# Optimization experiments

Measured on AMD Instinct MI355X. Metric: run time of the kernel, lower is better.

## Reference

```python
import jax, jax.numpy as jnp
import numpy as np

DIM = 768
NUM_HEADS = 12
HEAD_DIM = DIM // NUM_HEADS


def setup_inputs() -> dict:
    key = jax.random.key(0)
    k1, k2, k3 = jax.random.split(key, 3)
    B, N, C = 8, 4096, DIM
    x = jax.random.normal(k1, (B, N, C), dtype=jnp.float32)
    # torch nn.Linear weights are (out_features, in_features)
    W_qkv = jax.random.normal(k2, (3 * C, C), dtype=jnp.float32) * 0.02
    b_qkv = jnp.zeros((3 * C,), dtype=jnp.float32)
    W_proj = jax.random.normal(k3, (C, C), dtype=jnp.float32) * 0.02
    b_proj = jnp.zeros((C,), dtype=jnp.float32)
    return {"x": x, "W_qkv": W_qkv, "b_qkv": b_qkv, "W_proj": W_proj, "b_proj": b_proj}


def reference(x, W_qkv, b_qkv, W_proj, b_proj):
    B, N, C = x.shape
    H, D = NUM_HEADS, HEAD_DIM
    # qkv projection -> (3, B, H, N, D)
    qkv = (x @ W_qkv.T + b_qkv).reshape(B, N, 3, H, D).transpose(2, 0, 3, 1, 4)
    q, k, v = qkv[0], qkv[1], qkv[2]
    # feature map: elu(x) + 1 (positive kernel features)
    q = jax.nn.elu(q) + 1.0
    k = jax.nn.elu(k) + 1.0
    # kernelized linear attention: (K^T V) then Q (K^T V)
    kv = jnp.einsum('bhnd,bhnv->bhdv', k, v)          # (B,H,D,D)
    out = jnp.einsum('bhnd,bhdv->bhnv', q, kv)        # (B,H,N,D)
    k_sum = k.sum(axis=2)                             # (B,H,D)
    normalizer = jnp.einsum('bhnd,bhd->bhn', q, k_sum) + 1e-06
    out = out / normalizer[..., None]
    out = out.transpose(0, 2, 1, 3).reshape(B, N, C)
    out = out @ W_proj.T + b_proj
    return out
```

## Files before the change

### kernel.cpp

```cpp
#include <hip/hip_runtime.h>
#include <hip/hip_fp16.h>
#include <math.h>

#define NHEADS 12
#define SEQ 4096
#define BATCH 8

typedef _Float16 half8 __attribute__((ext_vector_type(8)));
typedef float floatx4 __attribute__((ext_vector_type(4)));

__global__ void zero_kernel(float* p, int n) {
  int i = blockIdx.x * 256 + threadIdx.x;
  if (i < n) p[i] = 0.f;
}

__global__ void cast_f2h(const float* __restrict__ in, __half* __restrict__ out, int n) {
  int i = (blockIdx.x * 256 + threadIdx.x) * 4;
  if (i < n) {
    float4 v = *(const float4*)&in[i];
    ushort4 o;
    o.x = __half_as_ushort(__float2half(v.x));
    o.y = __half_as_ushort(__float2half(v.y));
    o.z = __half_as_ushort(__float2half(v.z));
    o.w = __half_as_ushort(__float2half(v.w));
    *(ushort4*)&out[i] = o;
  }
}

__device__ __forceinline__ void stage_tile(const __half* __restrict__ gbase, int ldg,
                                           _Float16* lds, int t) {
#pragma unroll
  for (int it = 0; it < 2; ++it) {
    const int s  = it * 256 + t;
    const int mp = s >> 3, ps = s & 7;
    const int p  = ps ^ (mp & 7);
    const int r  = mp * 2 + (p >> 2);
    const int q  = p & 3;
    const __half* g = gbase + (size_t)r * ldg + q * 8;
    _Float16* dst = lds + (s >> 6) * 512;
    __builtin_amdgcn_global_load_lds((const __attribute__((address_space(1))) void*)g,
                                     (__attribute__((address_space(3))) void*)dst, 16, 0, 0);
  }
}
__device__ __forceinline__ void stage_blk(const __half* __restrict__ gbase, int ldg,
                                          _Float16* lds, int t) {
  const int mp = t >> 3, ps = t & 7;
  const int p  = ps ^ (mp & 7);
  const int r  = mp * 2 + (p >> 2);
  const int q  = p & 3;
  const __half* g = gbase + (size_t)r * ldg + q * 8;
  _Float16* dst = lds + (t >> 6) * 512;
  __builtin_amdgcn_global_load_lds((const __attribute__((address_space(1))) void*)g,
                                   (__attribute__((address_space(3))) void*)dst, 16, 0, 0);
}
__device__ __forceinline__ half8 read_frag(const _Float16* lds, int row, int quad) {
  const int mp = row >> 1;
  const int p  = ((row & 1) << 2) | quad;
  const int ps = p ^ (mp & 7);
  return *(const half8*)(lds + (mp * 8 + ps) * 8);
}

__device__ __forceinline__ void write_l64(_Float16* lds, int row, int col, float v) {
  lds[row * 64 + ((((col >> 3) ^ (row & 7))) << 3) + (col & 7)] = (_Float16)v;
}
__device__ __forceinline__ half8 read_l64c(const _Float16* lds, int row, int c) {
  return *(const half8*)(lds + row * 64 + ((c ^ (row & 7)) << 3));
}

__device__ __forceinline__ void barrier_raw() {
  asm volatile("s_barrier" ::: "memory");
}

template<int MODE>
__global__ __launch_bounds__(512, 2) void hgemm256_kernel(
    const __half* __restrict__ A, const __half* __restrict__ W,
    const float* __restrict__ bias,
    __half* __restrict__ outK, __half* __restrict__ outV,
    float* __restrict__ outF, int colBase)
{
  const int K = 768;
  const int NT = 24;
  extern __shared__ __align__(16) _Float16 sh[];
  const int t    = threadIdx.x;
  const int w    = t >> 6;
  const int l    = t & 63;
  const int quad = l >> 4;
  const int mrow = l & 15;
  const int wm   = w >> 2;
  const int wn   = w & 3;

  constexpr int JB = (MODE == 1) ? 6 : 3;
  const int bid  = blockIdx.x;
  const int xcd  = bid & 7;
  const int ii   = bid >> 3;
  const int mg   = ii / JB;
  const int jj   = ii - mg * JB;
  const int m0   = (xcd * 16 + mg) * 256;
  const int j0   = jj * 256;

  floatx4 acc[8][4];
#pragma unroll
  for (int i = 0; i < 8; ++i)
#pragma unroll
    for (int j = 0; j < 4; ++j) acc[i][j] = (floatx4){0.f, 0.f, 0.f, 0.f};

#pragma unroll
  for (int kt = 0; kt < 3; ++kt) {
    _Float16* db = sh + kt * 16384;
    const int kg = kt * 32;
    stage_blk(A + (size_t)m0 * K + kg, K, db, t);
    stage_blk(A + (size_t)(m0 + 128) * K + kg, K, db + 4096, t);
    stage_blk(W + (size_t)(colBase + j0) * K + kg, K, db + 8192, t);
    stage_blk(W + (size_t)(colBase + j0 + 128) * K + kg, K, db + 12288, t);
  }
  asm volatile("s_waitcnt vmcnt(8)" ::: "memory");
  barrier_raw();

#pragma unroll 4
  for (int kt = 0; kt < NT; ++kt) {
    const _Float16* bb = sh + (kt & 3) * 16384;
    const bool st = (kt + 3 < NT);
    _Float16* db = sh + ((kt + 3) & 3) * 16384;
    const int kg = (kt + 3) * 32;
    half8 af[4], bf[4];

#pragma unroll
    for (int j = 0; j < 4; ++j) {
      const int C = wn * 64 + j * 16 + mrow;
      bf[j] = read_frag(bb + 8192 + (C >> 7) * 4096, C & 127, quad);
    }
#pragma unroll
    for (int i = 0; i < 4; ++i)
      af[i] = read_frag(bb + wm * 4096, i * 16 + mrow, quad);
    if (st) {
      stage_blk(A + (size_t)m0 * K + kg, K, db, t);
      stage_blk(A + (size_t)(m0 + 128) * K + kg, K, db + 4096, t);
    }
#pragma unroll
    for (int i = 0; i < 4; ++i)
#pragma unroll
      for (int j = 0; j < 4; ++j)
        acc[i][j] = __builtin_amdgcn_mfma_f32_16x16x32_f16(af[i], bf[j], acc[i][j], 0, 0, 0);

#pragma unroll
    for (int i = 0; i < 4; ++i)
      af[i] = read_frag(bb + wm * 4096, (i + 4) * 16 + mrow, quad);
    if (st) {
      stage_blk(W + (size_t)(colBase + j0) * K + kg, K, db + 8192, t);
      stage_blk(W + (size_t)(colBase + j0 + 128) * K + kg, K, db + 12288, t);
    }
#pragma unroll
    for (int i = 0; i < 4; ++i)
#pragma unroll
      for (int j = 0; j < 4; ++j)
        acc[i + 4][j] = __builtin_amdgcn_mfma_f32_16x16x32_f16(af[i], bf[j], acc[i + 4][j], 0, 0, 0);

    if (kt < NT - 3)       asm volatile("s_waitcnt vmcnt(8)" ::: "memory");
    else if (kt == NT - 3) asm volatile("s_waitcnt vmcnt(4)" ::: "memory");
    else if (kt == NT - 2) asm volatile("s_waitcnt vmcnt(0)" ::: "memory");
    barrier_raw();
  }

  if (MODE == 0) {
#pragma unroll
    for (int j = 0; j < 4; ++j) {
      const int col = j0 + wn * 64 + j * 16 + mrow;
      const float bsv = bias[col];
#pragma unroll
      for (int i = 0; i < 8; ++i)
#pragma unroll
        for (int r = 0; r < 4; ++r) {
          const int m = m0 + wm * 128 + i * 16 + quad * 4 + r;
          outF[(size_t)m * 768 + col] = acc[i][j][r] + bsv;
        }
    }
    return;
  }

  const int col0 = colBase + j0 + wn * 64;
  const int t3   = col0 / 768;
  const int h    = (col0 - t3 * 768) >> 6;
  __half* dst    = (t3 == 1) ? outK : outV;
  const int m0w  = m0 + wm * 128;
  const int b_   = m0w >> 12;
  const int n0w  = m0w & 4095;
  _Float16* scr  = sh + w * 4096;
  const size_t gbT = (size_t)(b_ * NHEADS + h) * 64 * 4096;

#pragma unroll
  for (int hf = 0; hf < 2; ++hf) {
#pragma unroll
    for (int j = 0; j < 4; ++j) {
      const int col = j * 16 + mrow;
      const float bsv = bias[col0 + col];
#pragma unroll
      for (int ii2 = 0; ii2 < 4; ++ii2)
#pragma unroll
        for (int r = 0; r < 4; ++r) {
          const int row = ii2 * 16 + quad * 4 + r;
          float val = acc[hf * 4 + ii2][j][r] + bsv;
          if (t3 == 1) val = (val > 0.f) ? (val + 1.f) : expf(val);
          write_l64(scr, col, row, val);
        }
    }
    barrier_raw();
#pragma unroll
    for (int it = 0; it < 8; ++it) {
      const int dd = it * 8 + (l >> 3);
      const int c  = l & 7;
      half8 vv = read_l64c(scr, dd, c);
      *(half8*)((_Float16*)dst + gbT + (size_t)dd * 4096 + n0w + hf * 64 + c * 8) = vv;
    }
    barrier_raw();
  }
}

__global__ __launch_bounds__(256) void kv_mfma_kernel(
    const __half* __restrict__ kT, const __half* __restrict__ vT,
    float* __restrict__ kv, float* __restrict__ ksum)
{
  extern __shared__ float red[];
  float* ksr = red + 4 * 4096;
  const int bh = blockIdx.x;
  const int sp = blockIdx.y;
  const int t  = threadIdx.x;
  const int w  = t >> 6;
  const int l  = t & 63;
  const int quad = l >> 4;
  const int mrow = l & 15;
  const size_t base = (size_t)bh * 64 * 4096;
  const int n0 = sp * 1024 + w * 256;

  floatx4 acc[4][4];
  floatx4 ks[4];
#pragma unroll
  for (int i = 0; i < 4; ++i) {
    ks[i] = (floatx4){0.f, 0.f, 0.f, 0.f};
#pragma unroll
    for (int j = 0; j < 4; ++j) acc[i][j] = (floatx4){0.f, 0.f, 0.f, 0.f};
  }
  half8 ones;
#pragma unroll
  for (int e = 0; e < 8; ++e) ones[e] = (_Float16)1.0f;

  const __half* pk[4];
  const __half* pv[4];
#pragma unroll
  for (int i = 0; i < 4; ++i) {
    pk[i] = kT + base + (size_t)(i * 16 + mrow) * 4096 + n0 + quad * 8;
    pv[i] = vT + base + (size_t)(i * 16 + mrow) * 4096 + n0 + quad * 8;
  }

#pragma unroll
  for (int nn = 0; nn < 256; nn += 32) {
    half8 af[4], bf[4];
#pragma unroll
    for (int i = 0; i < 4; ++i) af[i] = *(const half8*)(pk[i] + nn);
#pragma unroll
    for (int j = 0; j < 4; ++j) bf[j] = *(const half8*)(pv[j] + nn);
#pragma unroll
    for (int i = 0; i < 4; ++i)
#pragma unroll
      for (int j = 0; j < 4; ++j)
        acc[i][j] = __builtin_amdgcn_mfma_f32_16x16x32_f16(af[i], bf[j], acc[i][j], 0, 0, 0);
#pragma unroll
    for (int i = 0; i < 4; ++i)
      ks[i] = __builtin_amdgcn_mfma_f32_16x16x32_f16(af[i], ones, ks[i], 0, 0, 0);
  }

  float* rw = red + w * 4096;
#pragma unroll
  for (int i = 0; i < 4; ++i)
#pragma unroll
    for (int j = 0; j < 4; ++j)
#pragma unroll
      for (int r = 0; r < 4; ++r)
        rw[(i * 16 + quad * 4 + r) * 64 + j * 16 + mrow] = acc[i][j][r];
  if (mrow == 0) {
#pragma unroll
    for (int i = 0; i < 4; ++i)
#pragma unroll
      for (int r = 0; r < 4; ++r)
        ksr[w * 64 + i * 16 + quad * 4 + r] = ks[i][r];
  }
  __syncthreads();
#pragma unroll
  for (int ii = 0; ii < 16; ++ii) {
    const int idx = ii * 256 + t;
    const float s = red[idx] + red[4096 + idx] + red[8192 + idx] + red[12288 + idx];
    atomicAdd(&kv[(size_t)bh * 4096 + idx], s);
  }
  if (t < 64)
    atomicAdd(&ksum[(size_t)bh * 64 + t], ksr[t] + ksr[64 + t] + ksr[128 + t] + ksr[192 + t]);
}

__global__ __launch_bounds__(256) void qattn_kernel(
    const __half* __restrict__ A, const __half* __restrict__ W,
    const float* __restrict__ bias,
    const float* __restrict__ kvg, const float* __restrict__ ksumg,
    __half* __restrict__ att)
{
  const int K = 768;
  __shared__ __align__(16) _Float16 sh[24576];
  _Float16* As = sh;
  _Float16* Bs = sh + 4096;
  __shared__ float norms[256];
  __shared__ float ksums[128];
  const int t    = threadIdx.x;
  const int w    = t >> 6;
  const int l    = t & 63;
  const int quad = l >> 4;
  const int mrow = l & 15;
  const int m0   = blockIdx.x * 128;
  const int j0   = blockIdx.y * 128;
  const int wr   = (w >> 1) * 64;
  const int wc   = (w & 1) * 64;
  const int b_   = m0 >> 12;
  const int h0   = j0 >> 6;

  {
    _Float16* kvT0 = sh + 16384;
#pragma unroll
    for (int ii = 0; ii < 32; ++ii) {
      const int gidx = ii * 256 + t;
      const int head = gidx >> 12;
      const int r    = gidx & 4095;
      const float val = kvg[(size_t)(b_ * NHEADS + h0 + head) * 4096 + r];
      write_l64(kvT0 + head * 4096, r & 63, r >> 6, val);
    }
    if (t < 128) ksums[t] = ksumg[(size_t)(b_ * NHEADS + h0 + (t >> 6)) * 64 + (t & 63)];
  }

  floatx4 acc[4][4];
#pragma unroll
  for (int i = 0; i < 4; ++i)
#pragma unroll
    for (int j = 0; j < 4; ++j) acc[i][j] = (floatx4){0.f, 0.f, 0.f, 0.f};

  for (int k0 = 0; k0 < K; k0 += 32) {
    __syncthreads();
    stage_tile(A + (size_t)m0 * K + k0, K, As, t);
    stage_tile(W + (size_t)j0 * K + k0, K, Bs, t);
    __syncthreads();
    half8 af[4], bf[4];
#pragma unroll
    for (int i = 0; i < 4; ++i) af[i] = read_frag(As, wr + i * 16 + mrow, quad);
#pragma unroll
    for (int j = 0; j < 4; ++j) bf[j] = read_frag(Bs, wc + j * 16 + mrow, quad);
#pragma unroll
    for (int i = 0; i < 4; ++i)
#pragma unroll
      for (int j = 0; j < 4; ++j)
        acc[i][j] = __builtin_amdgcn_mfma_f32_16x16x32_f16(af[i], bf[j], acc[i][j], 0, 0, 0);
  }

  _Float16* qtile = sh + w * 4096;
  const _Float16* kvT = sh + 16384 + (w & 1) * 4096;
  const int hh = w & 1;

  __syncthreads();
#pragma unroll
  for (int j = 0; j < 4; ++j) {
    const int col = j * 16 + mrow;
    const float bsv = bias[j0 + wc + col];
#pragma unroll
    for (int i = 0; i < 4; ++i)
#pragma unroll
      for (int r = 0; r < 4; ++r) {
        const int row = i * 16 + quad * 4 + r;
        float val = acc[i][j][r] + bsv;
        val = (val > 0.f) ? (val + 1.f) : expf(val);
        write_l64(qtile, row, col, val);
      }
  }
  __syncthreads();

  {
    float nrm = 0.f;
#pragma unroll
    for (int c = 0; c < 8; ++c) {
      half8 qv = read_l64c(qtile, l, c);
#pragma unroll
      for (int e = 0; e < 8; ++e) nrm += (float)qv[e] * ksums[hh * 64 + c * 8 + e];
    }
    norms[w * 64 + l] = 1.f / (nrm + 1e-6f);
  }

  floatx4 oacc[4][4];
#pragma unroll
  for (int i = 0; i < 4; ++i)
#pragma unroll
    for (int j = 0; j < 4; ++j) oacc[i][j] = (floatx4){0.f, 0.f, 0.f, 0.f};
#pragma unroll
  for (int ks = 0; ks < 2; ++ks) {
    half8 af[4], bf[4];
#pragma unroll
    for (int i = 0; i < 4; ++i) af[i] = read_l64c(qtile, i * 16 + mrow, ks * 4 + quad);
#pragma unroll
    for (int j = 0; j < 4; ++j) bf[j] = read_l64c(kvT, j * 16 + mrow, ks * 4 + quad);
#pragma unroll
    for (int i = 0; i < 4; ++i)
#pragma unroll
      for (int j = 0; j < 4; ++j)
        oacc[i][j] = __builtin_amdgcn_mfma_f32_16x16x32_f16(af[i], bf[j], oacc[i][j], 0, 0, 0);
  }
  __syncthreads();

#pragma unroll
  for (int i = 0; i < 4; ++i)
#pragma unroll
    for (int r = 0; r < 4; ++r) {
      const int row = i * 16 + quad * 4 + r;
      const float rn = norms[w * 64 + row];
#pragma unroll
      for (int j = 0; j < 4; ++j)
        write_l64(qtile, row, j * 16 + mrow, oacc[i][j][r] * rn);
    }
  __syncthreads();
  const int n0w = (m0 & 4095) + wr;
  const size_t abase = (size_t)(b_ * SEQ + n0w) * 768 + (h0 + hh) * 64;
#pragma unroll
  for (int it = 0; it < 8; ++it) {
    const int row = it * 8 + (l >> 3);
    const int c   = l & 7;
    half8 vv = read_l64c(qtile, row, c);
    *(half8*)((_Float16*)att + abase + (size_t)row * 768 + c * 8) = vv;
  }
}

extern "C" void kernel_launch(void* const* d_in, const int* in_sizes, int n_in,
                              void* d_out, int out_size, void* d_ws, size_t ws_size,
                              hipStream_t stream)
{
  const float* x     = (const float*)d_in[0];
  const float* Wqkv  = (const float*)d_in[1];
  const float* bqkv  = (const float*)d_in[2];
  const float* Wproj = (const float*)d_in[3];
  const float* bproj = (const float*)d_in[4];
  float* out = (float*)d_out;

  const size_t SZ = (size_t)BATCH * NHEADS * SEQ * 64;
  __half* xh  = (__half*)d_ws;
  __half* Wqh = xh + SZ;
  __half* Wph = Wqh + (size_t)2304 * 768;
  __half* R3  = Wph + (size_t)768 * 768;
  __half* R4  = R3 + SZ;
  float*  kvb = (float*)(R4 + SZ);
  float*  ksum = kvb + 96 * 64 * 64;

  static bool attr_set = false;
  if (!attr_set) {
    hipFuncSetAttribute((const void*)hgemm256_kernel<1>,
                        hipFuncAttributeMaxDynamicSharedMemorySize, 131072);
    hipFuncSetAttribute((const void*)hgemm256_kernel<0>,
                        hipFuncAttributeMaxDynamicSharedMemorySize, 131072);
    hipFuncSetAttribute((const void*)kv_mfma_kernel,
                        hipFuncAttributeMaxDynamicSharedMemorySize, 66560);
    attr_set = true;
  }

  zero_kernel<<<1560, 256, 0, stream>>>(kvb, 96 * 64 * 64 + 96 * 64);

  cast_f2h<<<(int)(SZ / 1024), 256, 0, stream>>>(x, xh, (int)SZ);
  cast_f2h<<<(2304 * 768) / 1024, 256, 0, stream>>>(Wqkv, Wqh, 2304 * 768);
  cast_f2h<<<(768 * 768) / 1024, 256, 0, stream>>>(Wproj, Wph, 768 * 768);

  hgemm256_kernel<1><<<768, 512, 131072, stream>>>(
      xh, Wqh, bqkv, R3, R4, nullptr, 768);

  kv_mfma_kernel<<<dim3(96, 4), 256, 66560, stream>>>(R3, R4, kvb, ksum);

  qattn_kernel<<<dim3(256, 6), 256, 0, stream>>>(
      xh, Wqh, bqkv, kvb, ksum, R3);

  hgemm256_kernel<0><<<384, 512, 131072, stream>>>(
      R3, Wph, bproj, nullptr, nullptr, out, 0);
}
```

Before: 440.9 us.

## Split GEMM template; add 128x128 triple-buffered projection GEMM and MFMA priority barriers

The templated 256x256 GEMM is split in two. The K/V projection kernel now adds an extra barrier and s_setprio around each MFMA half-step, so waves line up and the matrix cores get issue priority. The output projection gets its own kernel: 128x128 tiles, 256 threads, a triple-buffered static-LDS pipeline and 1536 blocks, giving more blocks per CU and better load balance than 384 large blocks. The smaller tiles trade this occupancy for less operand reuse, and the extra barriers in the KV GEMM can add stalls.

```diff
diff --git a/kernel.cpp b/kernel.cpp
--- a/kernel.cpp
+++ b/kernel.cpp
@@ -71,12 +71,10 @@
   asm volatile("s_barrier" ::: "memory");
 }
 
-template<int MODE>
-__global__ __launch_bounds__(512, 2) void hgemm256_kernel(
+__global__ __launch_bounds__(512, 2) void hgemm_kv8_kernel(
     const __half* __restrict__ A, const __half* __restrict__ W,
     const float* __restrict__ bias,
-    __half* __restrict__ outK, __half* __restrict__ outV,
-    float* __restrict__ outF, int colBase)
+    __half* __restrict__ outK, __half* __restrict__ outV)
 {
   const int K = 768;
   const int NT = 24;
@@ -89,12 +87,11 @@
   const int wm   = w >> 2;
   const int wn   = w & 3;
 
-  constexpr int JB = (MODE == 1) ? 6 : 3;
   const int bid  = blockIdx.x;
   const int xcd  = bid & 7;
   const int ii   = bid >> 3;
-  const int mg   = ii / JB;
-  const int jj   = ii - mg * JB;
+  const int mg   = ii / 6;
+  const int jj   = ii - mg * 6;
   const int m0   = (xcd * 16 + mg) * 256;
   const int j0   = jj * 256;
 
@@ -110,8 +107,8 @@
     const int kg = kt * 32;
     stage_blk(A + (size_t)m0 * K + kg, K, db, t);
     stage_blk(A + (size_t)(m0 + 128) * K + kg, K, db + 4096, t);
-    stage_blk(W + (size_t)(colBase + j0) * K + kg, K, db + 8192, t);
-    stage_blk(W + (size_t)(colBase + j0 + 128) * K + kg, K, db + 12288, t);
+    stage_blk(W + (size_t)(768 + j0) * K + kg, K, db + 8192, t);
+    stage_blk(W + (size_t)(768 + j0 + 128) * K + kg, K, db + 12288, t);
   }
   asm volatile("s_waitcnt vmcnt(8)" ::: "memory");
   barrier_raw();
@@ -136,24 +133,30 @@
       stage_blk(A + (size_t)m0 * K + kg, K, db, t);
       stage_blk(A + (size_t)(m0 + 128) * K + kg, K, db + 4096, t);
     }
+    barrier_raw();
+    __builtin_amdgcn_s_setprio(1);
 #pragma unroll
     for (int i = 0; i < 4; ++i)
 #pragma unroll
       for (int j = 0; j < 4; ++j)
         acc[i][j] = __builtin_amdgcn_mfma_f32_16x16x32_f16(af[i], bf[j], acc[i][j], 0, 0, 0);
+    __builtin_amdgcn_s_setprio(0);
 
 #pragma unroll
     for (int i = 0; i < 4; ++i)
       af[i] = read_frag(bb + wm * 4096, (i + 4) * 16 + mrow, quad);
     if (st) {
-      stage_blk(W + (size_t)(colBase + j0) * K + kg, K, db + 8192, t);
-      stage_blk(W + (size_t)(colBase + j0 + 128) * K + kg, K, db + 12288, t);
-    }
+      stage_blk(W + (size_t)(768 + j0) * K + kg, K, db + 8192, t);
+      stage_blk(W + (size_t)(768 + j0 + 128) * K + kg, K, db + 12288, t);
+    }
+    barrier_raw();
+    __builtin_amdgcn_s_setprio(1);
 #pragma unroll
     for (int i = 0; i < 4; ++i)
 #pragma unroll
       for (int j = 0; j < 4; ++j)
         acc[i + 4][j] = __builtin_amdgcn_mfma_f32_16x16x32_f16(af[i], bf[j], acc[i + 4][j], 0, 0, 0);
+    __builtin_amdgcn_s_setprio(0);
 
     if (kt < NT - 3)       asm volatile("s_waitcnt vmcnt(8)" ::: "memory");
     else if (kt == NT - 3) asm volatile("s_waitcnt vmcnt(4)" ::: "memory");
@@ -161,23 +164,7 @@
     barrier_raw();
   }
 
-  if (MODE == 0) {
-#pragma unroll
-    for (int j = 0; j < 4; ++j) {
-      const int col = j0 + wn * 64 + j * 16 + mrow;
-      const float bsv = bias[col];
-#pragma unroll
-      for (int i = 0; i < 8; ++i)
-#pragma unroll
-        for (int r = 0; r < 4; ++r) {
-          const int m = m0 + wm * 128 + i * 16 + quad * 4 + r;
-          outF[(size_t)m * 768 + col] = acc[i][j][r] + bsv;
-        }
-    }
-    return;
-  }
-
-  const int col0 = colBase + j0 + wn * 64;
+  const int col0 = 768 + j0 + wn * 64;
   const int t3   = col0 / 768;
   const int h    = (col0 - t3 * 768) >> 6;
   __half* dst    = (t3 == 1) ? outK : outV;
@@ -212,6 +199,86 @@
       *(half8*)((_Float16*)dst + gbT + (size_t)dd * 4096 + n0w + hf * 64 + c * 8) = vv;
     }
     barrier_raw();
+  }
+}
+
+__global__ __launch_bounds__(256, 3) void hgemm_proj_kernel(
+    const __half* __restrict__ A, const __half* __restrict__ W,
+    const float* __restrict__ bias, float* __restrict__ outF)
+{
+  const int K = 768;
+  const int NT = 24;
+  __shared__ __align__(16) _Float16 sh[3 * 8192];
+  const int t    = threadIdx.x;
+  const int w    = t >> 6;
+  const int l    = t & 63;
+  const int quad = l >> 4;
+  const int mrow = l & 15;
+  const int wr   = (w >> 1) * 64;
+  const int wc   = (w & 1) * 64;
+
+  const int bid  = blockIdx.x;
+  const int xcd  = bid & 7;
+  const int ii   = bid >> 3;
+  const int mg   = ii / 6;
+  const int jj   = ii - mg * 6;
+  const int m0   = (xcd * 32 + mg) * 128;
+  const int j0   = jj * 128;
+
+  floatx4 acc[4][4];
+#pragma unroll
+  for (int i = 0; i < 4; ++i)
+#pragma unroll
+    for (int j = 0; j < 4; ++j) acc[i][j] = (floatx4){0.f, 0.f, 0.f, 0.f};
+
+  stage_tile(A + (size_t)m0 * K + 0, K, sh + 0, t);
+  stage_tile(W + (size_t)j0 * K + 0, K, sh + 4096, t);
+  stage_tile(A + (size_t)m0 * K + 32, K, sh + 8192, t);
+  stage_tile(W + (size_t)j0 * K + 32, K, sh + 12288, t);
+  asm volatile("s_waitcnt vmcnt(4)" ::: "memory");
+  barrier_raw();
+
+  int cur = 0, nxt = 2;
+#pragma unroll 3
+  for (int kt = 0; kt < NT; ++kt) {
+    const _Float16* bb = sh + cur * 8192;
+    _Float16* db = sh + nxt * 8192;
+    const bool st = (kt + 2 < NT);
+    const int kg = (kt + 2) * 32;
+
+    if (st) {
+      stage_tile(A + (size_t)m0 * K + kg, K, db, t);
+      stage_tile(W + (size_t)j0 * K + kg, K, db + 4096, t);
+    }
+    half8 af[4], bf[4];
+#pragma unroll
+    for (int i = 0; i < 4; ++i) af[i] = read_frag(bb, wr + i * 16 + mrow, quad);
+#pragma unroll
+    for (int j = 0; j < 4; ++j) bf[j] = read_frag(bb + 4096, wc + j * 16 + mrow, quad);
+#pragma unroll
+    for (int i = 0; i < 4; ++i)
+#pragma unroll
+      for (int j = 0; j < 4; ++j)
+        acc[i][j] = __builtin_amdgcn_mfma_f32_16x16x32_f16(af[i], bf[j], acc[i][j], 0, 0, 0);
+
+    if (kt < NT - 2)       asm volatile("s_waitcnt vmcnt(4)" ::: "memory");
+    else if (kt == NT - 2) asm volatile("s_waitcnt vmcnt(0)" ::: "memory");
+    barrier_raw();
+    cur = (cur + 1) % 3;
+    nxt = (nxt + 1) % 3;
+  }
+
+#pragma unroll
+  for (int j = 0; j < 4; ++j) {
+    const int col = j0 + wc + j * 16 + mrow;
+    const float bsv = bias[col];
+#pragma unroll
+    for (int i = 0; i < 4; ++i)
+#pragma unroll
+      for (int r = 0; r < 4; ++r) {
+        const int m = m0 + wr + i * 16 + quad * 4 + r;
+        outF[(size_t)m * 768 + col] = acc[i][j][r] + bsv;
+      }
   }
 }
 
@@ -450,9 +517,7 @@
 
   static bool attr_set = false;
   if (!attr_set) {
-    hipFuncSetAttribute((const void*)hgemm256_kernel<1>,
-                        hipFuncAttributeMaxDynamicSharedMemorySize, 131072);
-    hipFuncSetAttribute((const void*)hgemm256_kernel<0>,
+    hipFuncSetAttribute((const void*)hgemm_kv8_kernel,
                         hipFuncAttributeMaxDynamicSharedMemorySize, 131072);
     hipFuncSetAttribute((const void*)kv_mfma_kernel,
                         hipFuncAttributeMaxDynamicSharedMemorySize, 66560);
@@ -465,14 +530,12 @@
   cast_f2h<<<(2304 * 768) / 1024, 256, 0, stream>>>(Wqkv, Wqh, 2304 * 768);
   cast_f2h<<<(768 * 768) / 1024, 256, 0, stream>>>(Wproj, Wph, 768 * 768);
 
-  hgemm256_kernel<1><<<768, 512, 131072, stream>>>(
-      xh, Wqh, bqkv, R3, R4, nullptr, 768);
+  hgemm_kv8_kernel<<<768, 512, 131072, stream>>>(xh, Wqh, bqkv, R3, R4);
 
   kv_mfma_kernel<<<dim3(96, 4), 256, 66560, stream>>>(R3, R4, kvb, ksum);
 
   qattn_kernel<<<dim3(256, 6), 256, 0, stream>>>(
       xh, Wqh, bqkv, kvb, ksum, R3);
 
-  hgemm256_kernel<0><<<384, 512, 131072, stream>>>(
-      R3, Wph, bproj, nullptr, nullptr, out, 0);
-}
+  hgemm_proj_kernel<<<1536, 256, 0, stream>>>(R3, Wph, bproj, out);
+}
```

New measurement: 445.5 us. Within noise of the previous version (+1.1%).
